# Kernel tuning notes

Hardware: AMD Instinct MI355X
Metric: run time of the kernel (lower is better)

## Reference

```python
import jax, jax.numpy as jnp
import numpy as np

N_NODES = 100000
N_EDGES = 3200000
IN_DIM = 128
EMB = 32
NUM_GRAPHS = 256


def setup_inputs() -> dict:
    key = jax.random.key(0)
    ks = jax.random.split(key, 7)
    x = jax.random.normal(ks[0], (N_NODES, IN_DIM), dtype=jnp.float32)
    edge_index = jax.random.randint(ks[1], (2, N_EDGES), 0, N_NODES, dtype=jnp.int64)
    batch_index = jnp.sort(jax.random.randint(ks[2], (N_NODES,), 0, NUM_GRAPHS, dtype=jnp.int64))
    W1 = jax.random.normal(ks[3], (IN_DIM, EMB), dtype=jnp.float32) * (1.0 / np.sqrt(IN_DIM))
    b1 = jax.random.normal(ks[4], (EMB,), dtype=jnp.float32) * 0.01
    Wout = jax.random.normal(ks[5], (2 * EMB, 1), dtype=jnp.float32) * (1.0 / np.sqrt(2 * EMB))
    bout = jax.random.normal(ks[6], (1,), dtype=jnp.float32) * 0.01
    return {"x": x, "edge_index": edge_index, "batch_index": batch_index,
            "W1": W1, "b1": b1, "Wout": Wout, "bout": bout}


def gcn_conv(x, edge_index, W, b):
    """PyG GCNConv: add self-loops, symmetric deg^-1/2 normalization, XW, scatter-add, +bias."""
    N = x.shape[0]
    xw = x @ W  # [N, out]
    src, dst = edge_index[0], edge_index[1]
    # degree includes self-loop (+1)
    deg = jax.ops.segment_sum(jnp.ones(src.shape[0], dtype=xw.dtype), dst, num_segments=N) + 1.0
    dinv = jax.lax.rsqrt(deg)  # deg >= 1 so safe
    norm = dinv[src] * dinv[dst]  # [E]
    msg = xw[src] * norm[:, None]  # [E, out]
    agg = jax.ops.segment_sum(msg, dst, num_segments=N)
    # self-loop contribution: dinv[i]^2 * xw[i]
    agg = agg + xw * (dinv * dinv)[:, None]
    return agg + b


def reference(x, edge_index, batch_index, W1, b1, Wout, bout):
    h = gcn_conv(x, edge_index, W1, b1)           # [N, EMB]
    h = jnp.tanh(h)
    sums = jax.ops.segment_sum(h, batch_index, num_segments=NUM_GRAPHS)   # global_add_pool
    counts = jax.ops.segment_sum(jnp.ones((h.shape[0],), dtype=h.dtype), batch_index, num_segments=NUM_GRAPHS)
    means = sums / jnp.maximum(counts, 1.0)[:, None]                       # global_mean_pool
    pooled = jnp.concatenate([sums, means], axis=1)  # [G, 2*EMB]
    return pooled @ Wout + bout                      # [G, 1]
```

## Files before the change

kernel.cpp:

```cpp
#include <hip/hip_runtime.h>
#include <hip/hip_fp16.h>

#define N_NODES    100000
#define N_EDGES    3200000
#define IN_DIM     128
#define EMB        32
#define NUM_GRAPHS 256

#define FB         1024
#define NODES_PB   128
#define NBUCKETS   782
#define F1_EPB     20000
#define F1_BLOCKS  160
#define H_EPB      20000
#define H_BLOCKS   160
#define XW_BLOCKS  1563
#define CAP        5632

typedef _Float16 half8 __attribute__((ext_vector_type(8)));
typedef float floatx4 __attribute__((ext_vector_type(4)));

__global__ __launch_bounds__(512) void k_hist1(const int* __restrict__ ei,
                                               int* __restrict__ chist) {
    __shared__ int h[FB];
    int t = threadIdx.x;
    for (int i = t; i < FB; i += 512) h[i] = 0;
    __syncthreads();
    int e0 = blockIdx.x * H_EPB;
    int e1 = e0 + H_EPB; if (e1 > N_EDGES) e1 = N_EDGES;
    for (int e = e0 + t; e < e1; e += 512)
        atomicAdd(&h[ei[N_EDGES + e] >> 7], 1);
    __syncthreads();
    for (int i = t; i < FB; i += 512)
        if (h[i]) atomicAdd(&chist[i], h[i]);
}

__global__ __launch_bounds__(512) void k_aux(const int* __restrict__ chist,
                                             int* __restrict__ cbase,
                                             int* __restrict__ gcursor,
                                             const int* __restrict__ batch,
                                             float* __restrict__ sums,
                                             float* __restrict__ counts) {
    int t = threadIdx.x;
    if (blockIdx.x == 0) {
        __shared__ int ts[512];
        int v0 = chist[2 * t], v1 = chist[2 * t + 1];
        int tot = v0 + v1;
        ts[t] = tot;
        __syncthreads();
        for (int off = 1; off < 512; off <<= 1) {
            int u = (t >= off) ? ts[t - off] : 0;
            __syncthreads();
            ts[t] += u;
            __syncthreads();
        }
        int base = ts[t] - tot;
        cbase[2 * t] = base;          gcursor[2 * t] = base;
        cbase[2 * t + 1] = base + v0; gcursor[2 * t + 1] = base + v0;
        if (t == 511) cbase[FB] = ts[511];
    } else {
        for (int i = t; i < NUM_GRAPHS * EMB; i += 512) sums[i] = 0.f;
        if (t < NUM_GRAPHS) {
            int lo = 0, hi = N_NODES;
            while (lo < hi) { int mid = (lo + hi) >> 1; if (batch[mid] < t) lo = mid + 1; else hi = mid; }
            int a = lo;
            lo = 0; hi = N_NODES;
            int g1 = t + 1;
            while (lo < hi) { int mid = (lo + hi) >> 1; if (batch[mid] < g1) lo = mid + 1; else hi = mid; }
            counts[t] = (float)(lo - a);
        }
    }
}

__global__ __launch_bounds__(512) void k_fill1(const int* __restrict__ ei,
                                               int* __restrict__ gcursor,
                                               unsigned int* __restrict__ recs) {
    __shared__ int hist[FB];
    __shared__ int base[FB];
    __shared__ int lcur[FB];
    int t = threadIdx.x;
    for (int i = t; i < FB; i += 512) { hist[i] = 0; lcur[i] = 0; }
    __syncthreads();
    int e0 = blockIdx.x * F1_EPB;
    int e1 = e0 + F1_EPB; if (e1 > N_EDGES) e1 = N_EDGES;
    for (int e = e0 + t; e < e1; e += 512)
        atomicAdd(&hist[ei[N_EDGES + e] >> 7], 1);
    __syncthreads();
    for (int i = t; i < FB; i += 512)
        if (hist[i]) base[i] = atomicAdd(&gcursor[i], hist[i]);
    __syncthreads();
    for (int e = e0 + t; e < e1; e += 512) {
        int s = ei[e];
        int d = ei[N_EDGES + e];
        int b = d >> 7;
        int pos = base[b] + atomicAdd(&lcur[b], 1);
        recs[pos] = ((unsigned int)(d & 127) << 24) | (unsigned int)s;
    }
}

__global__ __launch_bounds__(512) void k_fill2(const unsigned int* __restrict__ recs,
                                               const int* __restrict__ cbase,
                                               int* __restrict__ edge_src,
                                               int* __restrict__ rowstart,
                                               float* __restrict__ dinv) {
    __shared__ unsigned int lbuf[CAP];
    __shared__ int h2[NODES_PB], cur2[NODES_PB], sc[NODES_PB];
    int t = threadIdx.x, b = blockIdx.x;
    if (t < NODES_PB) h2[t] = 0;
    __syncthreads();
    int seg0 = cbase[b];
    int cnt = cbase[b + 1] - seg0;
    for (int j = t; j < cnt; j += 512) {
        unsigned int r = recs[seg0 + j];
        if (j < CAP) lbuf[j] = r;
        atomicAdd(&h2[r >> 24], 1);
    }
    __syncthreads();
    int v = 0;
    if (t < NODES_PB) { v = h2[t]; sc[t] = v; }
    __syncthreads();
    for (int off = 1; off < NODES_PB; off <<= 1) {
        int u = 0;
        if (t < NODES_PB && t >= off) u = sc[t - off];
        __syncthreads();
        if (t < NODES_PB) sc[t] += u;
        __syncthreads();
    }
    int node0 = b << 7;
    if (t < NODES_PB) {
        int excl = sc[t] - v;
        cur2[t] = excl;
        int node = node0 + t;
        if (node < N_NODES) {
            rowstart[node] = seg0 + excl;
            dinv[node] = rsqrtf((float)v + 1.0f);
        }
    }
    if (b == 0 && t == 0) rowstart[N_NODES] = N_EDGES;
    __syncthreads();
    for (int j = t; j < cnt; j += 512) {
        unsigned int r = (j < CAP) ? lbuf[j] : recs[seg0 + j];
        int p = atomicAdd(&cur2[r >> 24], 1);
        edge_src[seg0 + p] = (int)(r & 0x00FFFFFF);
    }
}

__global__ __launch_bounds__(256) void k_xw(const float* __restrict__ x,
                                            const float* __restrict__ W1,
                                            const float* __restrict__ dinv,
                                            __half* __restrict__ xwh) {
    __shared__ _Float16 Wh[IN_DIM * (EMB + 1)];
    for (int i = threadIdx.x; i < IN_DIM * EMB; i += 256)
        Wh[(i >> 5) * (EMB + 1) + (i & 31)] = (_Float16)W1[i];
    __syncthreads();
    int wave = threadIdx.x >> 6;
    int lane = threadIdx.x & 63;
    int m = lane & 15, quad = lane >> 4;
    int row0 = (blockIdx.x * 4 + wave) * 16;
    if (row0 >= N_NODES) return;
    half8 bfrag[2][4];
#pragma unroll
    for (int nt = 0; nt < 2; ++nt)
#pragma unroll
        for (int ks = 0; ks < 4; ++ks)
#pragma unroll
            for (int j = 0; j < 8; ++j)
                bfrag[nt][ks][j] = Wh[(ks * 32 + quad * 8 + j) * (EMB + 1) + nt * 16 + m];
    const float* xr = x + (size_t)(row0 + m) * IN_DIM + quad * 8;
    floatx4 c0 = {0.f, 0.f, 0.f, 0.f}, c1 = {0.f, 0.f, 0.f, 0.f};
#pragma unroll
    for (int ks = 0; ks < 4; ++ks) {
        float4 a0 = *(const float4*)(xr + ks * 32);
        float4 a1 = *(const float4*)(xr + ks * 32 + 4);
        half8 af;
        af[0] = (_Float16)a0.x; af[1] = (_Float16)a0.y;
        af[2] = (_Float16)a0.z; af[3] = (_Float16)a0.w;
        af[4] = (_Float16)a1.x; af[5] = (_Float16)a1.y;
        af[6] = (_Float16)a1.z; af[7] = (_Float16)a1.w;
        c0 = __builtin_amdgcn_mfma_f32_16x16x32_f16(af, bfrag[0][ks], c0, 0, 0, 0);
        c1 = __builtin_amdgcn_mfma_f32_16x16x32_f16(af, bfrag[1][ks], c1, 0, 0, 0);
    }
#pragma unroll
    for (int r = 0; r < 4; ++r) {
        int ro = row0 + quad * 4 + r;
        float di = dinv[ro];
        xwh[(size_t)ro * EMB + m]      = __float2half(c0[r] * di);
        xwh[(size_t)ro * EMB + 16 + m] = __float2half(c1[r] * di);
    }
}

template<int K>
__device__ __forceinline__ void gstep(const int* __restrict__ es,
                                      const __half2* __restrict__ rows,
                                      int cc, int e, float& a0, float& a1) {
    int s[K];
    float2 f[K];
#pragma unroll
    for (int k = 0; k < K; ++k) s[k] = es[e + k];
#pragma unroll
    for (int k = 0; k < K; ++k) f[k] = __half22float2(rows[s[k] * 16 + cc]);
#pragma unroll
    for (int k = 0; k < K; ++k) { a0 += f[k].x; a1 += f[k].y; }
}

__global__ __launch_bounds__(256) void k_gather(const __half* __restrict__ xws,
                                                const float* __restrict__ dinv,
                                                const int* __restrict__ rowstart,
                                                const int* __restrict__ edge_src,
                                                const int* __restrict__ batch,
                                                const float* __restrict__ b1,
                                                float* __restrict__ sums) {
    const __half2* rows = (const __half2*)xws;
    int grp = threadIdx.x >> 4;
    int cc  = threadIdx.x & 15;
    int i = blockIdx.x * 16 + grp;
    float di = dinv[i];
    int e0 = rowstart[i], e1 = rowstart[i + 1];
    float a0 = 0.f, a1 = 0.f;
    int e = e0;
    for (; e + 16 <= e1; e += 16) gstep<16>(edge_src, rows, cc, e, a0, a1);
    if (e + 8 <= e1) { gstep<8>(edge_src, rows, cc, e, a0, a1); e += 8; }
    if (e + 4 <= e1) { gstep<4>(edge_src, rows, cc, e, a0, a1); e += 4; }
    if (e + 2 <= e1) { gstep<2>(edge_src, rows, cc, e, a0, a1); e += 2; }
    if (e < e1)      { gstep<1>(edge_src, rows, cc, e, a0, a1); }
    float2 fs = __half22float2(rows[i * 16 + cc]);
    float2 bb = *(const float2*)(b1 + 2 * cc);
    float h0 = tanhf((a0 + fs.x) * di + bb.x);
    float h1 = tanhf((a1 + fs.y) * di + bb.y);

    __shared__ float hs[16][EMB];
    __shared__ int gb[16];
    *(float2*)&hs[grp][2 * cc] = make_float2(h0, h1);
    if (cc == 0) gb[grp] = batch[i];
    __syncthreads();
    if (threadIdx.x < 32) {
        int col = threadIdx.x;
        int rr = 0;
        while (rr < 16) {
            int g0 = gb[rr];
            float a = hs[rr][col];
            int r2 = rr + 1;
            while (r2 < 16 && gb[r2] == g0) { a += hs[r2][col]; ++r2; }
            atomicAdd(&sums[g0 * EMB + col], a);
            rr = r2;
        }
    }
}

__global__ __launch_bounds__(64) void k_out(const float* __restrict__ sums,
                                            const float* __restrict__ counts,
                                            const float* __restrict__ Wout,
                                            const float* __restrict__ bout,
                                            float* __restrict__ out) {
    int g = blockIdx.x * 64 + threadIdx.x;
    if (g >= NUM_GRAPHS) return;
    float inv = 1.0f / fmaxf(counts[g], 1.0f);
    float acc = bout[0];
#pragma unroll
    for (int c = 0; c < EMB; ++c) {
        float s = sums[g * EMB + c];
        acc += s * Wout[c] + s * inv * Wout[EMB + c];
    }
    out[g] = acc;
}

extern "C" void kernel_launch(void* const* d_in, const int* in_sizes, int n_in,
                              void* d_out, int out_size, void* d_ws, size_t ws_size,
                              hipStream_t stream) {
    const float* x     = (const float*)d_in[0];
    const int*   ei    = (const int*)d_in[1];
    const int*   batch = (const int*)d_in[2];
    const float* W1    = (const float*)d_in[3];
    const float* b1    = (const float*)d_in[4];
    const float* Wout  = (const float*)d_in[5];
    const float* bout  = (const float*)d_in[6];
    float* out = (float*)d_out;

    char* ws = (char*)d_ws;
    __half* xwh        = (__half*)ws;       ws += (size_t)N_NODES * EMB * sizeof(__half);
    unsigned int* recs = (unsigned int*)ws; ws += (size_t)N_EDGES * sizeof(int);
    int*   edge_src    = (int*)ws;          ws += (size_t)N_EDGES * sizeof(int);
    int*   rowstart    = (int*)ws;          ws += (size_t)(N_NODES + 4) * sizeof(int);
    float* dinv        = (float*)ws;        ws += (size_t)N_NODES * sizeof(float);
    int*   chist       = (int*)ws;          ws += FB * sizeof(int);
    int*   cbase       = (int*)ws;          ws += (FB + 2) * sizeof(int);
    int*   gcursor     = (int*)ws;          ws += FB * sizeof(int);
    float* sums        = (float*)ws;        ws += (size_t)NUM_GRAPHS * EMB * sizeof(float);
    float* counts      = (float*)ws;

    hipMemsetAsync(chist, 0, FB * sizeof(int), stream);

    k_hist1 <<<H_BLOCKS, 512, 0, stream>>>(ei, chist);
    k_aux   <<<2, 512, 0, stream>>>(chist, cbase, gcursor, batch, sums, counts);
    k_fill1 <<<F1_BLOCKS, 512, 0, stream>>>(ei, gcursor, recs);
    k_fill2 <<<NBUCKETS, 512, 0, stream>>>(recs, cbase, edge_src, rowstart, dinv);
    k_xw    <<<XW_BLOCKS, 256, 0, stream>>>(x, W1, dinv, xwh);
    k_gather<<<N_NODES / 16, 256, 0, stream>>>(xwh, dinv, rowstart, edge_src, batch, b1, sums);
    k_out   <<<(NUM_GRAPHS + 63) / 64, 64, 0, stream>>>(sums, counts, Wout, bout, out);
}
```

Baseline: 228.6 us.

## Replace global-atomic bucket cursors with per-block histogram matrix and column scan

The edge bucketing pass now writes a per-block histogram matrix (512 blocks x 1024 buckets) instead of atomically accumulating a global histogram. A new column-scan kernel computes exclusive per-block offsets, so the fill kernel no longer recomputes its histogram or uses global atomics on cursors. The grid also grows from 160 to 512 blocks for more parallelism. In exchange it adds a 2 MB intermediate matrix, an extra kernel launch, and a serial column scan that only 16 blocks of 64 threads perform.

```diff
diff --git a/kernel.cpp b/kernel.cpp
--- a/kernel.cpp
+++ b/kernel.cpp
@@ -10,56 +10,67 @@
 #define FB         1024
 #define NODES_PB   128
 #define NBUCKETS   782
-#define F1_EPB     20000
-#define F1_BLOCKS  160
-#define H_EPB      20000
-#define H_BLOCKS   160
+#define HB         512
+#define HB_EPB     6250
 #define XW_BLOCKS  1563
 #define CAP        5632
 
 typedef _Float16 half8 __attribute__((ext_vector_type(8)));
 typedef float floatx4 __attribute__((ext_vector_type(4)));
 
-__global__ __launch_bounds__(512) void k_hist1(const int* __restrict__ ei,
-                                               int* __restrict__ chist) {
+__global__ __launch_bounds__(512) void k_hist(const int* __restrict__ ei,
+                                              int* __restrict__ H) {
     __shared__ int h[FB];
     int t = threadIdx.x;
     for (int i = t; i < FB; i += 512) h[i] = 0;
     __syncthreads();
-    int e0 = blockIdx.x * H_EPB;
-    int e1 = e0 + H_EPB; if (e1 > N_EDGES) e1 = N_EDGES;
+    int e0 = blockIdx.x * HB_EPB;
+    int e1 = e0 + HB_EPB;
     for (int e = e0 + t; e < e1; e += 512)
         atomicAdd(&h[ei[N_EDGES + e] >> 7], 1);
     __syncthreads();
-    for (int i = t; i < FB; i += 512)
-        if (h[i]) atomicAdd(&chist[i], h[i]);
-}
-
-__global__ __launch_bounds__(512) void k_aux(const int* __restrict__ chist,
-                                             int* __restrict__ cbase,
-                                             int* __restrict__ gcursor,
-                                             const int* __restrict__ batch,
-                                             float* __restrict__ sums,
-                                             float* __restrict__ counts) {
+    int* row = H + (size_t)blockIdx.x * FB;
+    for (int i = t; i < FB; i += 512) row[i] = h[i];
+}
+
+__global__ __launch_bounds__(64) void k_colscan(int* __restrict__ H,
+                                                int* __restrict__ chist) {
+    int c = blockIdx.x * 64 + threadIdx.x;
+    int run = 0;
+    for (int b = 0; b < HB; b += 4) {
+        int i0 = (b + 0) * FB + c, i1 = (b + 1) * FB + c;
+        int i2 = (b + 2) * FB + c, i3 = (b + 3) * FB + c;
+        int v0 = H[i0], v1 = H[i1], v2 = H[i2], v3 = H[i3];
+        H[i0] = run;
+        H[i1] = run + v0;
+        H[i2] = run + v0 + v1;
+        H[i3] = run + v0 + v1 + v2;
+        run += v0 + v1 + v2 + v3;
+    }
+    chist[c] = run;
+}
+
+__global__ __launch_bounds__(1024) void k_aux(const int* __restrict__ chist,
+                                              int* __restrict__ cbase,
+                                              const int* __restrict__ batch,
+                                              float* __restrict__ sums,
+                                              float* __restrict__ counts) {
     int t = threadIdx.x;
     if (blockIdx.x == 0) {
-        __shared__ int ts[512];
-        int v0 = chist[2 * t], v1 = chist[2 * t + 1];
-        int tot = v0 + v1;
-        ts[t] = tot;
+        __shared__ int ts[FB];
+        int v = chist[t];
+        ts[t] = v;
         __syncthreads();
-        for (int off = 1; off < 512; off <<= 1) {
+        for (int off = 1; off < FB; off <<= 1) {
             int u = (t >= off) ? ts[t - off] : 0;
             __syncthreads();
             ts[t] += u;
             __syncthreads();
         }
-        int base = ts[t] - tot;
-        cbase[2 * t] = base;          gcursor[2 * t] = base;
-        cbase[2 * t + 1] = base + v0; gcursor[2 * t + 1] = base + v0;
-        if (t == 511) cbase[FB] = ts[511];
+        cbase[t] = ts[t] - v;
+        if (t == FB - 1) cbase[FB] = ts[FB - 1];
     } else {
-        for (int i = t; i < NUM_GRAPHS * EMB; i += 512) sums[i] = 0.f;
+        for (int i = t; i < NUM_GRAPHS * EMB; i += 1024) sums[i] = 0.f;
         if (t < NUM_GRAPHS) {
             int lo = 0, hi = N_NODES;
             while (lo < hi) { int mid = (lo + hi) >> 1; if (batch[mid] < t) lo = mid + 1; else hi = mid; }
@@ -72,28 +83,21 @@
     }
 }
 
-__global__ __launch_bounds__(512) void k_fill1(const int* __restrict__ ei,
-                                               int* __restrict__ gcursor,
-                                               unsigned int* __restrict__ recs) {
-    __shared__ int hist[FB];
-    __shared__ int base[FB];
+__global__ __launch_bounds__(512) void k_fill(const int* __restrict__ ei,
+                                              const int* __restrict__ H,
+                                              const int* __restrict__ cbase,
+                                              unsigned int* __restrict__ recs) {
     __shared__ int lcur[FB];
     int t = threadIdx.x;
-    for (int i = t; i < FB; i += 512) { hist[i] = 0; lcur[i] = 0; }
-    __syncthreads();
-    int e0 = blockIdx.x * F1_EPB;
-    int e1 = e0 + F1_EPB; if (e1 > N_EDGES) e1 = N_EDGES;
-    for (int e = e0 + t; e < e1; e += 512)
-        atomicAdd(&hist[ei[N_EDGES + e] >> 7], 1);
-    __syncthreads();
-    for (int i = t; i < FB; i += 512)
-        if (hist[i]) base[i] = atomicAdd(&gcursor[i], hist[i]);
-    __syncthreads();
+    const int* row = H + (size_t)blockIdx.x * FB;
+    for (int i = t; i < FB; i += 512) lcur[i] = cbase[i] + row[i];
+    __syncthreads();
+    int e0 = blockIdx.x * HB_EPB;
+    int e1 = e0 + HB_EPB;
     for (int e = e0 + t; e < e1; e += 512) {
         int s = ei[e];
         int d = ei[N_EDGES + e];
-        int b = d >> 7;
-        int pos = base[b] + atomicAdd(&lcur[b], 1);
+        int pos = atomicAdd(&lcur[d >> 7], 1);
         recs[pos] = ((unsigned int)(d & 127) << 24) | (unsigned int)s;
     }
 }
@@ -280,21 +284,20 @@
     __half* xwh        = (__half*)ws;       ws += (size_t)N_NODES * EMB * sizeof(__half);
     unsigned int* recs = (unsigned int*)ws; ws += (size_t)N_EDGES * sizeof(int);
     int*   edge_src    = (int*)ws;          ws += (size_t)N_EDGES * sizeof(int);
+    int*   H           = (int*)ws;          ws += (size_t)HB * FB * sizeof(int);
     int*   rowstart    = (int*)ws;          ws += (size_t)(N_NODES + 4) * sizeof(int);
     float* dinv        = (float*)ws;        ws += (size_t)N_NODES * sizeof(float);
     int*   chist       = (int*)ws;          ws += FB * sizeof(int);
     int*   cbase       = (int*)ws;          ws += (FB + 2) * sizeof(int);
-    int*   gcursor     = (int*)ws;          ws += FB * sizeof(int);
     float* sums        = (float*)ws;        ws += (size_t)NUM_GRAPHS * EMB * sizeof(float);
     float* counts      = (float*)ws;
 
-    hipMemsetAsync(chist, 0, FB * sizeof(int), stream);
-
-    k_hist1 <<<H_BLOCKS, 512, 0, stream>>>(ei, chist);
-    k_aux   <<<2, 512, 0, stream>>>(chist, cbase, gcursor, batch, sums, counts);
-    k_fill1 <<<F1_BLOCKS, 512, 0, stream>>>(ei, gcursor, recs);
-    k_fill2 <<<NBUCKETS, 512, 0, stream>>>(recs, cbase, edge_src, rowstart, dinv);
-    k_xw    <<<XW_BLOCKS, 256, 0, stream>>>(x, W1, dinv, xwh);
-    k_gather<<<N_NODES / 16, 256, 0, stream>>>(xwh, dinv, rowstart, edge_src, batch, b1, sums);
-    k_out   <<<(NUM_GRAPHS + 63) / 64, 64, 0, stream>>>(sums, counts, Wout, bout, out);
-}
+    k_hist   <<<HB, 512, 0, stream>>>(ei, H);
+    k_colscan<<<FB / 64, 64, 0, stream>>>(H, chist);
+    k_aux    <<<2, 1024, 0, stream>>>(chist, cbase, batch, sums, counts);
+    k_fill   <<<HB, 512, 0, stream>>>(ei, H, cbase, recs);
+    k_fill2  <<<NBUCKETS, 512, 0, stream>>>(recs, cbase, edge_src, rowstart, dinv);
+    k_xw     <<<XW_BLOCKS, 256, 0, stream>>>(x, W1, dinv, xwh);
+    k_gather <<<N_NODES / 16, 256, 0, stream>>>(xwh, dinv, rowstart, edge_src, batch, b1, sums);
+    k_out    <<<(NUM_GRAPHS + 63) / 64, 64, 0, stream>>>(sums, counts, Wout, bout, out);
+}
```

After: 233.7 us. +2.2%, slower.
